# Performance work log

Measured on AMD Instinct MI355X. Metric: run time of the kernel, lower is better.

Reference implementation:

```python
import jax, jax.numpy as jnp
import numpy as np

N = 100_000      # total nodes (entities + relations)
D = 128          # embed_dim
E_ER = 1_000_000 # entity->relation edges
E_EE = 500_000   # entity->entity edges


def setup_inputs() -> dict:
    key = jax.random.key(0)
    ks = jax.random.split(key, 14)
    s = 0.05
    return {
        "node_emb": jax.random.normal(ks[0], (N, D), jnp.float32),
        "er_src": jax.random.randint(ks[1], (E_ER,), 0, N),
        "er_dst": jax.random.randint(ks[2], (E_ER,), 0, N),
        "ee_src": jax.random.randint(ks[3], (E_EE,), 0, N),
        "ee_dst": jax.random.randint(ks[4], (E_EE,), 0, N),
        "ee_weight": jax.random.uniform(ks[5], (E_EE,), jnp.float32),
        # learned params (stored as (in, out) so y = x @ W + b)
        "W_attn_w": jax.random.normal(ks[6], (2 * D, D), jnp.float32) * s,
        "W_attn_b": jax.random.normal(ks[7], (D,), jnp.float32) * s,
        "w0_w": jax.random.normal(ks[8], (D,), jnp.float32) * s,
        "w0_b": jax.random.normal(ks[9], (), jnp.float32) * s,
        "W_self_w": jax.random.normal(ks[10], (D, D), jnp.float32) * s,
        "W_self_b": jax.random.normal(ks[11], (D,), jnp.float32) * s,
        "W_neigh_w": jax.random.normal(ks[12], (D, D), jnp.float32) * s,
        "W_neigh_b": jax.random.normal(ks[13], (D,), jnp.float32) * s,
    }


def _segment_softmax(values, seg_ids, num_segments):
    # torch scatter_reduce_ starts from zeros with include_self=True -> max includes 0
    seg_max = jnp.maximum(
        jax.ops.segment_max(values, seg_ids, num_segments=num_segments), 0.0)
    exp_v = jnp.exp(values - seg_max[seg_ids])
    seg_sum = jax.ops.segment_sum(exp_v, seg_ids, num_segments=num_segments)
    return exp_v / (seg_sum[seg_ids] + 1e-9)


def reference(node_emb, er_src, er_dst, ee_src, ee_dst, ee_weight,
              W_attn_w, W_attn_b, w0_w, w0_b, W_self_w, W_self_b,
              W_neigh_w, W_neigh_b):
    n = node_emb.shape[0]
    # --- entity -> relation attention messages ---
    h_emb = node_emb[er_src]                      # (E, D)
    r_emb = node_emb[er_dst]                      # (E, D)
    pair = jnp.concatenate([r_emb, h_emb], axis=-1)  # (E, 2D)
    e_ij = jnp.tanh(pair @ W_attn_w + W_attn_b) @ w0_w + w0_b  # (E,)
    attn = _segment_softmax(e_ij, er_src, n)      # (E,)
    r_msg = r_emb @ W_neigh_w + W_neigh_b         # (E, D)
    agg = jnp.zeros_like(node_emb).at[er_src].add(attn[:, None] * r_msg)
    # --- entity -> entity weighted messages (note: scatter index is ee_src, as in source) ---
    src_emb = node_emb[ee_src]                    # (E2, D)
    ee_msg = src_emb @ W_neigh_w + W_neigh_b
    agg = agg.at[ee_src].add(ee_weight[:, None] * ee_msg)
    # --- self update ---
    return jnp.tanh(node_emb @ W_self_w + W_self_b + agg)
```

## Files before the change

### kernel.cpp

```cpp
#include <hip/hip_runtime.h>

#define DD 128

typedef short s16x8 __attribute__((ext_vector_type(8)));
typedef float f32x4 __attribute__((ext_vector_type(4)));

__device__ __forceinline__ float tanh_fast(float x) {
  float e = __expf(2.0f * x);
  return 1.0f - 2.0f / (e + 1.0f);
}

__device__ __forceinline__ unsigned short f2bf(float f) {
  unsigned u = __float_as_uint(f);
  u += 0x7FFFu + ((u >> 16) & 1u);
  return (unsigned short)(u >> 16);
}

__device__ __forceinline__ float bf2f(unsigned short u) {
  return __uint_as_float(((unsigned)u) << 16);
}

extern "C" __global__ __launch_bounds__(256) void k_tobf(
    const float* __restrict__ emb, unsigned short* __restrict__ ebf, int total8) {
  int i = blockIdx.x * 256 + threadIdx.x;
  if (i >= total8) return;
  const float4* e4 = (const float4*)emb;
  float4 x = e4[(size_t)i * 2];
  float4 y = e4[(size_t)i * 2 + 1];
  uint4 o;
  o.x = (unsigned)f2bf(x.x) | ((unsigned)f2bf(x.y) << 16);
  o.y = (unsigned)f2bf(x.z) | ((unsigned)f2bf(x.w) << 16);
  o.z = (unsigned)f2bf(y.x) | ((unsigned)f2bf(y.y) << 16);
  o.w = (unsigned)f2bf(y.z) | ((unsigned)f2bf(y.w) << 16);
  *(uint4*)(ebf + (size_t)i * 8) = o;
}

extern "C" __global__ __launch_bounds__(256) void k_packw1(
    const float* __restrict__ Wattn, unsigned short* __restrict__ WB) {
  int t = blockIdx.x * 256 + threadIdx.x;
  int lane = t & 63;
  int cks = t >> 6;
  int ks = cks & 3, ct = cks >> 2;
  int c = ct * 16 + (lane & 15);
  int kb = ks * 32 + ((lane >> 4) << 3);
  const float* srcp = (c < DD) ? (Wattn + (size_t)kb * DD + c)
                               : (Wattn + (size_t)(DD + kb) * DD + (c - DD));
  unsigned short* dst = WB + (size_t)t * 8;
#pragma unroll
  for (int j = 0; j < 8; ++j) dst[j] = f2bf(srcp[(size_t)j * DD]);
}

extern "C" __global__ __launch_bounds__(256) void k_packw2(
    const float* __restrict__ Wself, const float* __restrict__ Wneigh,
    unsigned short* __restrict__ WBh, unsigned short* __restrict__ WBl) {
  int t = blockIdx.x * 256 + threadIdx.x;
  int lane = t & 63;
  int cks = t >> 6;
  int ks = cks & 7, ct = cks >> 3;
  int c = ct * 16 + (lane & 15);
  int k0 = ks * 32 + ((lane >> 4) << 3);
#pragma unroll
  for (int j = 0; j < 8; ++j) {
    int k = k0 + j;
    float v = (k < DD) ? Wself[(size_t)k * DD + c] : Wneigh[(size_t)(k - DD) * DD + c];
    unsigned short h = f2bf(v);
    float r = v - bf2f(h);
    WBh[(size_t)t * 8 + j] = h;
    WBl[(size_t)t * 8 + j] = f2bf(r);
  }
}

extern "C" __global__ __launch_bounds__(256) void k_pq_mfma(
    const unsigned short* __restrict__ ebf, const unsigned short* __restrict__ WB,
    const float* __restrict__ battn, unsigned short* __restrict__ PQ, int n) {
  const int wave = threadIdx.x >> 6, lane = threadIdx.x & 63;
  const int v0 = blockIdx.x * 64 + wave * 16;
  const int row = v0 + (lane & 15);
  const int kb = (lane >> 4) << 3;
  const bool rok = row < n;
  const s16x8 zf = {0, 0, 0, 0, 0, 0, 0, 0};
  s16x8 a[4];
#pragma unroll
  for (int ks = 0; ks < 4; ++ks)
    a[ks] = rok ? *(const s16x8*)(ebf + (size_t)row * DD + ks * 32 + kb) : zf;
  f32x4 acc[16];
#pragma unroll
  for (int ct = 0; ct < 16; ++ct) acc[ct] = (f32x4)(0.f);
  const s16x8* wb = (const s16x8*)WB;
#pragma unroll
  for (int ct = 0; ct < 16; ++ct) {
#pragma unroll
    for (int ks = 0; ks < 4; ++ks) {
      s16x8 b = wb[(ct * 4 + ks) * 64 + lane];
      acc[ct] = __builtin_amdgcn_mfma_f32_16x16x32_bf16(a[ks], b, acc[ct], 0, 0, 0);
    }
  }
  const int r0 = (lane >> 4) << 2;
  const int col0 = lane & 15;
#pragma unroll
  for (int ct = 0; ct < 16; ++ct) {
    int c = ct * 16 + col0;
    float bias = (c < DD) ? battn[c] : 0.f;
#pragma unroll
    for (int r = 0; r < 4; ++r) {
      int v = v0 + r0 + r;
      if (v < n) PQ[(size_t)v * 256 + c] = f2bf(acc[ct][r] + bias);
    }
  }
}

extern "C" __global__ __launch_bounds__(256) void k_hist(
    const int* __restrict__ src, int* __restrict__ count, int nE) {
  int e = blockIdx.x * 256 + threadIdx.x;
  if (e < nE) atomicAdd(&count[src[e]], 1);
}

extern "C" __global__ __launch_bounds__(256) void k_scan(
    const int* __restrict__ in, int* __restrict__ outp,
    int* __restrict__ bsum, int n) {
  __shared__ int s[512];
  __shared__ int total;
  const int t = threadIdx.x;
  const int base = blockIdx.x * 512;
  for (int i = t; i < 512; i += 256) s[i] = (base + i < n) ? in[base + i] : 0;
  __syncthreads();
  for (int d = 1; d < 512; d <<= 1) {
    int stride = d * 2;
    int nidx = 512 / stride;
    if (t < nidx) {
      int idx = (t + 1) * stride - 1;
      s[idx] += s[idx - d];
    }
    __syncthreads();
  }
  if (t == 0) { total = s[511]; s[511] = 0; }
  __syncthreads();
  for (int d = 256; d >= 1; d >>= 1) {
    int stride = d * 2;
    int nidx = 512 / stride;
    if (t < nidx) {
      int idx = (t + 1) * stride - 1;
      int tmp = s[idx - d];
      s[idx - d] = s[idx];
      s[idx] += tmp;
    }
    __syncthreads();
  }
  for (int i = t; i < 512; i += 256)
    if (base + i < n) outp[base + i] = s[i];
  if (t == 0) bsum[blockIdx.x] = total;
}

extern "C" __global__ __launch_bounds__(256) void k_scan_add(
    int* __restrict__ off, const int* __restrict__ bofs, int n, int total) {
  int base = blockIdx.x * 512;
  int add = bofs[blockIdx.x];
  for (int i = threadIdx.x; i < 512; i += 256) {
    int idx = base + i;
    if (idx < n) off[idx] += add;
  }
  if (blockIdx.x == 0 && threadIdx.x == 0) off[n] = total;
}

extern "C" __global__ __launch_bounds__(256) void k_eij_scatter(
    const unsigned short* __restrict__ PQ,
    const int* __restrict__ src, const int* __restrict__ dstp,
    const float* __restrict__ w0w, const float* __restrict__ w0b,
    int* __restrict__ off_mut, float* __restrict__ eij_s,
    int* __restrict__ dst_s, int nE) {
  int t = blockIdx.x * 256 + threadIdx.x;
  int e = t >> 4;
  if (e >= nE) return;
  int lane = t & 15;
  int s = src[e], d = dstp[e];
  uint4 pv = *(const uint4*)(PQ + (size_t)d * 256 + lane * 8);
  uint4 qv = *(const uint4*)(PQ + (size_t)s * 256 + DD + lane * 8);
  float4 wa = *(const float4*)&w0w[lane * 8];
  float4 wbv = *(const float4*)&w0w[lane * 8 + 4];
  unsigned pw[4] = {pv.x, pv.y, pv.z, pv.w};
  unsigned qw[4] = {qv.x, qv.y, qv.z, qv.w};
  float wv[8] = {wa.x, wa.y, wa.z, wa.w, wbv.x, wbv.y, wbv.z, wbv.w};
  float acc = 0.f;
#pragma unroll
  for (int j = 0; j < 8; ++j) {
    unsigned up = (j & 1) ? (pw[j >> 1] & 0xFFFF0000u) : (pw[j >> 1] << 16);
    unsigned uq = (j & 1) ? (qw[j >> 1] & 0xFFFF0000u) : (qw[j >> 1] << 16);
    float x = __uint_as_float(up) + __uint_as_float(uq);
    acc = fmaf(tanh_fast(x), wv[j], acc);
  }
  acc += __shfl_xor(acc, 8);
  acc += __shfl_xor(acc, 4);
  acc += __shfl_xor(acc, 2);
  acc += __shfl_xor(acc, 1);
  if (lane == 0) {
    float sv = acc + w0b[0];
    int pos = atomicAdd(&off_mut[s], 1);
    eij_s[pos] = sv;
    dst_s[pos] = d;
  }
}

extern "C" __global__ __launch_bounds__(256) void k_agg(
    const unsigned short* __restrict__ ebf, const int* __restrict__ off,
    const int* __restrict__ dst_s, const float* __restrict__ eij_s,
    float* __restrict__ U, float* __restrict__ ssum, int n) {
  int v = (blockIdx.x * 256 + threadIdx.x) >> 6;
  int lane = threadIdx.x & 63;
  if (v >= n) return;
  int start = off[v], end = off[v + 1];
  float m = 0.0f;
  for (int i = start + lane; i < end; i += 64) m = fmaxf(m, eij_s[i]);
#pragma unroll
  for (int o = 32; o; o >>= 1) m = fmaxf(m, __shfl_xor(m, o));
  float a0 = 0.f, a1 = 0.f, ssv = 0.f;
  for (int base = start; base < end; base += 64) {
    int i = base + lane;
    int dl = 0;
    float evl = 0.f;
    if (i < end) {
      dl = dst_s[i];
      evl = __expf(eij_s[i] - m);
    }
    int cnt = min(64, end - base);
    for (int j = 0; j < cnt; ++j) {
      int d = __shfl(dl, j);
      float ev = __shfl(evl, j);
      ssv += ev;
      unsigned x = *(const unsigned*)(ebf + (size_t)d * DD + lane * 2);
      a0 = fmaf(ev, bf2f((unsigned short)(x & 0xFFFFu)), a0);
      a1 = fmaf(ev, bf2f((unsigned short)(x >> 16)), a1);
    }
  }
  float2* U2 = (float2*)U;
  U2[(size_t)v * 64 + lane] = make_float2(a0, a1);
  if (lane == 0) ssum[v] = ssv;
}

extern "C" __global__ __launch_bounds__(256) void k_deg(
    const int* __restrict__ src, const float* __restrict__ wgt,
    float* __restrict__ g, int nE) {
  int e = blockIdx.x * 256 + threadIdx.x;
  if (e < nE) unsafeAtomicAdd(&g[src[e]], wgt[e]);
}

extern "C" __global__ __launch_bounds__(256) void k_out_mfma(
    const float* __restrict__ emb, const float* __restrict__ U,
    const float* __restrict__ ssum, const float* __restrict__ g,
    const unsigned short* __restrict__ WBh, const unsigned short* __restrict__ WBl,
    const float* __restrict__ bself, const float* __restrict__ bneigh,
    float* __restrict__ out, int n) {
  const int wave = threadIdx.x >> 6, lane = threadIdx.x & 63;
  const int v0 = blockIdx.x * 64 + wave * 16;
  const int row = v0 + (lane & 15);
  const int kb = (lane >> 4) << 3;
  const bool rok = row < n;
  float inv = 0.f, gv = 0.f;
  if (rok) {
    float sv = ssum[row];
    inv = 1.f / (sv + 1e-9f);
    gv = g[row];
  }
  s16x8 ah[8], al[8];
#pragma unroll
  for (int ks = 0; ks < 8; ++ks) {
    int k0 = (ks & 3) * 32 + kb;
    float x[8] = {0.f, 0.f, 0.f, 0.f, 0.f, 0.f, 0.f, 0.f};
    if (rok) {
      float4 ea = *(const float4*)(emb + (size_t)row * DD + k0);
      float4 eb = *(const float4*)(emb + (size_t)row * DD + k0 + 4);
      x[0] = ea.x; x[1] = ea.y; x[2] = ea.z; x[3] = ea.w;
      x[4] = eb.x; x[5] = eb.y; x[6] = eb.z; x[7] = eb.w;
      if (ks >= 4) {
        float4 ua = *(const float4*)(U + (size_t)row * DD + k0);
        float4 ub = *(const float4*)(U + (size_t)row * DD + k0 + 4);
        x[0] = fmaf(gv, x[0], ua.x * inv);
        x[1] = fmaf(gv, x[1], ua.y * inv);
        x[2] = fmaf(gv, x[2], ua.z * inv);
        x[3] = fmaf(gv, x[3], ua.w * inv);
        x[4] = fmaf(gv, x[4], ub.x * inv);
        x[5] = fmaf(gv, x[5], ub.y * inv);
        x[6] = fmaf(gv, x[6], ub.z * inv);
        x[7] = fmaf(gv, x[7], ub.w * inv);
      }
    }
    unsigned short hh[8], ll[8];
#pragma unroll
    for (int j = 0; j < 8; ++j) {
      unsigned short h = f2bf(x[j]);
      hh[j] = h;
      ll[j] = f2bf(x[j] - bf2f(h));
    }
    ah[ks] = *(const s16x8*)hh;
    al[ks] = *(const s16x8*)ll;
  }
  f32x4 acc[8];
#pragma unroll
  for (int ct = 0; ct < 8; ++ct) acc[ct] = (f32x4)(0.f);
  const s16x8* wbh = (const s16x8*)WBh;
  const s16x8* wbl = (const s16x8*)WBl;
#pragma unroll
  for (int ct = 0; ct < 8; ++ct) {
#pragma unroll
    for (int ks = 0; ks < 8; ++ks) {
      s16x8 bh = wbh[(ct * 8 + ks) * 64 + lane];
      s16x8 bl = wbl[(ct * 8 + ks) * 64 + lane];
      acc[ct] = __builtin_amdgcn_mfma_f32_16x16x32_bf16(ah[ks], bh, acc[ct], 0, 0, 0);
      acc[ct] = __builtin_amdgcn_mfma_f32_16x16x32_bf16(al[ks], bh, acc[ct], 0, 0, 0);
      acc[ct] = __builtin_amdgcn_mfma_f32_16x16x32_bf16(ah[ks], bl, acc[ct], 0, 0, 0);
    }
  }
  const int r0 = (lane >> 4) << 2;
  const int col0 = lane & 15;
  float tgr[4];
#pragma unroll
  for (int r = 0; r < 4; ++r) {
    int v = v0 + r0 + r;
    float tg = 0.f;
    if (v < n) {
      float sv = ssum[v];
      tg = sv / (sv + 1e-9f) + g[v];
    }
    tgr[r] = tg;
  }
#pragma unroll
  for (int ct = 0; ct < 8; ++ct) {
    int c = ct * 16 + col0;
    float bs = bself[c], bn = bneigh[c];
#pragma unroll
    for (int r = 0; r < 4; ++r) {
      int v = v0 + r0 + r;
      if (v < n) out[(size_t)v * DD + c] = tanh_fast(acc[ct][r] + bs + tgr[r] * bn);
    }
  }
}

static inline size_t al16(size_t x) { return (x + 15) & ~(size_t)15; }

extern "C" void kernel_launch(void* const* d_in, const int* in_sizes, int n_in,
                              void* d_out, int out_size, void* d_ws, size_t ws_size,
                              hipStream_t stream) {
  const float* emb = (const float*)d_in[0];
  const int* er_src = (const int*)d_in[1];
  const int* er_dst = (const int*)d_in[2];
  const int* ee_src = (const int*)d_in[3];
  const float* ee_w = (const float*)d_in[5];
  const float* Wattn = (const float*)d_in[6];
  const float* battn = (const float*)d_in[7];
  const float* w0w = (const float*)d_in[8];
  const float* w0b = (const float*)d_in[9];
  const float* Wself = (const float*)d_in[10];
  const float* bself = (const float*)d_in[11];
  const float* Wneigh = (const float*)d_in[12];
  const float* bneigh = (const float*)d_in[13];
  const int n = in_sizes[0] / DD;
  const int nER = in_sizes[1];
  const int nEE = in_sizes[3];

  char* w = (char*)d_ws;
  size_t o = 0;
  unsigned short* ebf = (unsigned short*)(w + o); o += al16((size_t)n * DD * 2);
  unsigned short* PQ  = (unsigned short*)(w + o);
  float* U = (float*)(w + o);                     o += al16((size_t)n * 256 * 2);
  int* dst_s = (int*)(w + o);   o += al16((size_t)nER * 4);
  float* eij_s = (float*)(w + o); o += al16((size_t)nER * 4);
  int* count = (int*)(w + o);   o += al16((size_t)n * 4);
  float* g = (float*)(w + o);   o += al16((size_t)n * 4);
  int* off = (int*)(w + o);     o += al16((size_t)(n + 4) * 4);
  int* off_mut = (int*)(w + o); o += al16((size_t)n * 4);
  float* ssum = (float*)(w + o); o += al16((size_t)n * 4);
  unsigned short* WB = (unsigned short*)(w + o);   o += 65536;
  unsigned short* WB2h = (unsigned short*)(w + o); o += 65536;
  unsigned short* WB2l = (unsigned short*)(w + o); o += 65536;
  int* bsum = (int*)(w + o);    o += 4096;
  int* dummy = (int*)(w + o);   o += 64;

  const int nb = (n + 511) / 512;
  const int total8 = n * DD / 8;

  hipMemsetAsync(count, 0, (size_t)n * 8, stream);

  k_tobf<<<(total8 + 255) / 256, 256, 0, stream>>>(emb, ebf, total8);
  k_packw1<<<16, 256, 0, stream>>>(Wattn, WB);
  k_packw2<<<16, 256, 0, stream>>>(Wself, Wneigh, WB2h, WB2l);
  k_pq_mfma<<<(n + 63) / 64, 256, 0, stream>>>(ebf, WB, battn, PQ, n);
  k_hist<<<(nER + 255) / 256, 256, 0, stream>>>(er_src, count, nER);
  k_scan<<<nb, 256, 0, stream>>>(count, off, bsum, n);
  k_scan<<<1, 256, 0, stream>>>(bsum, bsum, dummy, nb);
  k_scan_add<<<nb, 256, 0, stream>>>(off, bsum, n, nER);
  hipMemcpyAsync(off_mut, off, (size_t)n * 4, hipMemcpyDeviceToDevice, stream);
  k_eij_scatter<<<(nER * 16 + 255) / 256, 256, 0, stream>>>(
      PQ, er_src, er_dst, w0w, w0b, off_mut, eij_s, dst_s, nER);
  k_agg<<<(n + 3) / 4, 256, 0, stream>>>(ebf, off, dst_s, eij_s, U, ssum, n);
  k_deg<<<(nEE + 255) / 256, 256, 0, stream>>>(ee_src, ee_w, g, nEE);
  k_out_mfma<<<(n + 63) / 64, 256, 0, stream>>>(emb, U, ssum, g, WB2h, WB2l,
                                                bself, bneigh, (float*)d_out, n);
}
```

Before: 402.2 us.

## Fuse attention-score computation into aggregation with online softmax

The per-edge attention score is no longer computed in a separate scatter kernel. Each node's wave now computes the score for every incident edge itself, using a per-node fp32 Q row and gathered P rows, and keeps a running max and rescaling (online softmax) while accumulating. This removes the eij_s buffer, its write and re-read, and the per-edge Q gathers, and it shrinks the CSR scatter to destination indices only. In exchange, each edge iteration becomes a serial chain of dependent loads, tanh, a 6-step wave reduction and an exp, which may make the aggregation loop more latency-bound.

```diff
diff --git a/kernel.cpp b/kernel.cpp
--- a/kernel.cpp
+++ b/kernel.cpp
@@ -72,7 +72,8 @@
 
 extern "C" __global__ __launch_bounds__(256) void k_pq_mfma(
     const unsigned short* __restrict__ ebf, const unsigned short* __restrict__ WB,
-    const float* __restrict__ battn, unsigned short* __restrict__ PQ, int n) {
+    const float* __restrict__ battn, unsigned short* __restrict__ P,
+    float* __restrict__ Qf, int n) {
   const int wave = threadIdx.x >> 6, lane = threadIdx.x & 63;
   const int v0 = blockIdx.x * 64 + wave * 16;
   const int row = v0 + (lane & 15);
@@ -100,11 +101,13 @@
 #pragma unroll
   for (int ct = 0; ct < 16; ++ct) {
     int c = ct * 16 + col0;
-    float bias = (c < DD) ? battn[c] : 0.f;
 #pragma unroll
     for (int r = 0; r < 4; ++r) {
       int v = v0 + r0 + r;
-      if (v < n) PQ[(size_t)v * 256 + c] = f2bf(acc[ct][r] + bias);
+      if (v < n) {
+        if (c < DD) P[(size_t)v * DD + c] = f2bf(acc[ct][r] + battn[c]);
+        else Qf[(size_t)v * DD + (c - DD)] = acc[ct][r];
+      }
     }
   }
 }
@@ -162,74 +165,52 @@
   if (blockIdx.x == 0 && threadIdx.x == 0) off[n] = total;
 }
 
-extern "C" __global__ __launch_bounds__(256) void k_eij_scatter(
-    const unsigned short* __restrict__ PQ,
+extern "C" __global__ __launch_bounds__(256) void k_scatter_dst(
     const int* __restrict__ src, const int* __restrict__ dstp,
-    const float* __restrict__ w0w, const float* __restrict__ w0b,
-    int* __restrict__ off_mut, float* __restrict__ eij_s,
-    int* __restrict__ dst_s, int nE) {
-  int t = blockIdx.x * 256 + threadIdx.x;
-  int e = t >> 4;
+    int* __restrict__ off_mut, int* __restrict__ dst_s, int nE) {
+  int e = blockIdx.x * 256 + threadIdx.x;
   if (e >= nE) return;
-  int lane = t & 15;
-  int s = src[e], d = dstp[e];
-  uint4 pv = *(const uint4*)(PQ + (size_t)d * 256 + lane * 8);
-  uint4 qv = *(const uint4*)(PQ + (size_t)s * 256 + DD + lane * 8);
-  float4 wa = *(const float4*)&w0w[lane * 8];
-  float4 wbv = *(const float4*)&w0w[lane * 8 + 4];
-  unsigned pw[4] = {pv.x, pv.y, pv.z, pv.w};
-  unsigned qw[4] = {qv.x, qv.y, qv.z, qv.w};
-  float wv[8] = {wa.x, wa.y, wa.z, wa.w, wbv.x, wbv.y, wbv.z, wbv.w};
-  float acc = 0.f;
-#pragma unroll
-  for (int j = 0; j < 8; ++j) {
-    unsigned up = (j & 1) ? (pw[j >> 1] & 0xFFFF0000u) : (pw[j >> 1] << 16);
-    unsigned uq = (j & 1) ? (qw[j >> 1] & 0xFFFF0000u) : (qw[j >> 1] << 16);
-    float x = __uint_as_float(up) + __uint_as_float(uq);
-    acc = fmaf(tanh_fast(x), wv[j], acc);
-  }
-  acc += __shfl_xor(acc, 8);
-  acc += __shfl_xor(acc, 4);
-  acc += __shfl_xor(acc, 2);
-  acc += __shfl_xor(acc, 1);
-  if (lane == 0) {
-    float sv = acc + w0b[0];
-    int pos = atomicAdd(&off_mut[s], 1);
-    eij_s[pos] = sv;
-    dst_s[pos] = d;
-  }
-}
-
-extern "C" __global__ __launch_bounds__(256) void k_agg(
+  int pos = atomicAdd(&off_mut[src[e]], 1);
+  dst_s[pos] = dstp[e];
+}
+
+extern "C" __global__ __launch_bounds__(256) void k_fused(
+    const unsigned short* __restrict__ P, const float* __restrict__ Qf,
     const unsigned short* __restrict__ ebf, const int* __restrict__ off,
-    const int* __restrict__ dst_s, const float* __restrict__ eij_s,
-    float* __restrict__ U, float* __restrict__ ssum, int n) {
+    const int* __restrict__ dst_s, const float* __restrict__ w0w,
+    const float* __restrict__ w0b, float* __restrict__ U,
+    float* __restrict__ ssum, int n) {
   int v = (blockIdx.x * 256 + threadIdx.x) >> 6;
   int lane = threadIdx.x & 63;
   if (v >= n) return;
-  int start = off[v], end = off[v + 1];
+  const int start = off[v], end = off[v + 1];
+  float2 q = *(const float2*)(Qf + (size_t)v * DD + lane * 2);
+  float2 w = *(const float2*)(w0w + lane * 2);
+  const float wb = w0b[0];
   float m = 0.0f;
-  for (int i = start + lane; i < end; i += 64) m = fmaxf(m, eij_s[i]);
-#pragma unroll
-  for (int o = 32; o; o >>= 1) m = fmaxf(m, __shfl_xor(m, o));
-  float a0 = 0.f, a1 = 0.f, ssv = 0.f;
-  for (int base = start; base < end; base += 64) {
-    int i = base + lane;
-    int dl = 0;
-    float evl = 0.f;
-    if (i < end) {
-      dl = dst_s[i];
-      evl = __expf(eij_s[i] - m);
-    }
-    int cnt = min(64, end - base);
-    for (int j = 0; j < cnt; ++j) {
-      int d = __shfl(dl, j);
-      float ev = __shfl(evl, j);
-      ssv += ev;
-      unsigned x = *(const unsigned*)(ebf + (size_t)d * DD + lane * 2);
-      a0 = fmaf(ev, bf2f((unsigned short)(x & 0xFFFFu)), a0);
-      a1 = fmaf(ev, bf2f((unsigned short)(x >> 16)), a1);
-    }
+  float ssv = 0.f, a0 = 0.f, a1 = 0.f;
+  for (int i = start; i < end; ++i) {
+    int d = dst_s[i];
+    unsigned pe = *(const unsigned*)(P + (size_t)d * DD + lane * 2);
+    unsigned ee = *(const unsigned*)(ebf + (size_t)d * DD + lane * 2);
+    float x0 = bf2f((unsigned short)(pe & 0xFFFFu)) + q.x;
+    float x1 = bf2f((unsigned short)(pe >> 16)) + q.y;
+    float part = tanh_fast(x0) * w.x + tanh_fast(x1) * w.y;
+#pragma unroll
+    for (int o = 32; o; o >>= 1) part += __shfl_xor(part, o);
+    float s = part + wb;
+    float p;
+    if (s > m) {
+      float sc = __expf(m - s);
+      a0 *= sc; a1 *= sc; ssv *= sc;
+      m = s;
+      p = 1.0f;
+    } else {
+      p = __expf(s - m);
+    }
+    ssv += p;
+    a0 = fmaf(p, bf2f((unsigned short)(ee & 0xFFFFu)), a0);
+    a1 = fmaf(p, bf2f((unsigned short)(ee >> 16)), a1);
   }
   float2* U2 = (float2*)U;
   U2[(size_t)v * 64 + lane] = make_float2(a0, a1);
@@ -359,10 +340,11 @@
   char* w = (char*)d_ws;
   size_t o = 0;
   unsigned short* ebf = (unsigned short*)(w + o); o += al16((size_t)n * DD * 2);
-  unsigned short* PQ  = (unsigned short*)(w + o);
-  float* U = (float*)(w + o);                     o += al16((size_t)n * 256 * 2);
+  unsigned short* P   = (unsigned short*)(w + o); o += al16((size_t)n * DD * 2);
+  float* Qf = (float*)(w + o);
+  float* U  = Qf;
+  o += al16((size_t)n * DD * 4);
   int* dst_s = (int*)(w + o);   o += al16((size_t)nER * 4);
-  float* eij_s = (float*)(w + o); o += al16((size_t)nER * 4);
   int* count = (int*)(w + o);   o += al16((size_t)n * 4);
   float* g = (float*)(w + o);   o += al16((size_t)n * 4);
   int* off = (int*)(w + o);     o += al16((size_t)(n + 4) * 4);
@@ -382,15 +364,16 @@
   k_tobf<<<(total8 + 255) / 256, 256, 0, stream>>>(emb, ebf, total8);
   k_packw1<<<16, 256, 0, stream>>>(Wattn, WB);
   k_packw2<<<16, 256, 0, stream>>>(Wself, Wneigh, WB2h, WB2l);
-  k_pq_mfma<<<(n + 63) / 64, 256, 0, stream>>>(ebf, WB, battn, PQ, n);
+  k_pq_mfma<<<(n + 63) / 64, 256, 0, stream>>>(ebf, WB, battn, P, Qf, n);
   k_hist<<<(nER + 255) / 256, 256, 0, stream>>>(er_src, count, nER);
   k_scan<<<nb, 256, 0, stream>>>(count, off, bsum, n);
   k_scan<<<1, 256, 0, stream>>>(bsum, bsum, dummy, nb);
   k_scan_add<<<nb, 256, 0, stream>>>(off, bsum, n, nER);
   hipMemcpyAsync(off_mut, off, (size_t)n * 4, hipMemcpyDeviceToDevice, stream);
-  k_eij_scatter<<<(nER * 16 + 255) / 256, 256, 0, stream>>>(
-      PQ, er_src, er_dst, w0w, w0b, off_mut, eij_s, dst_s, nER);
-  k_agg<<<(n + 3) / 4, 256, 0, stream>>>(ebf, off, dst_s, eij_s, U, ssum, n);
+  k_scatter_dst<<<(nER + 255) / 256, 256, 0, stream>>>(er_src, er_dst, off_mut,
+                                                       dst_s, nER);
+  k_fused<<<(n + 3) / 4, 256, 0, stream>>>(P, Qf, ebf, off, dst_s, w0w, w0b,
+                                           U, ssum, n);
   k_deg<<<(nEE + 255) / 256, 256, 0, stream>>>(ee_src, ee_w, g, nEE);
   k_out_mfma<<<(n + 63) / 64, 256, 0, stream>>>(emb, U, ssum, g, WB2h, WB2l,
                                                 bself, bneigh, (float*)d_out, n);
```

Result: slower. 447.6 us (+11.3%).
